# Optimization experiments

Hardware: AMD Instinct MI355X
Metric: run time of the kernel (lower is better)

The kernel has to match this reference:

```python
import jax, jax.numpy as jnp
import numpy as np

ALPHA = 0.2      # LeakyReLU negative slope
NEG_INF = -9e15  # mask value from the original code

def setup_inputs() -> dict:
    key = jax.random.key(0)
    k1, k2, k3, k4 = jax.random.split(key, 4)
    B, M, F_IN, F_OUT = 16, 2048, 128, 64
    h = jax.random.normal(k1, (B, M, F_IN), dtype=jnp.float32)
    adj = jax.random.randint(k2, (B, M, M), 0, 2, dtype=jnp.int32)
    W = jax.random.normal(k3, (F_IN, F_OUT), dtype=jnp.float32) * 0.1
    a = jax.random.normal(k4, (2 * F_OUT, 1), dtype=jnp.float32) * 0.1
    return {"h": h, "adj": adj, "W": W, "a": a}

def reference(h, adj, W, a):
    # h: [B,M,Fin], adj: [B,M,M], W: [Fin,E], a: [2E,1]
    Wh = jnp.matmul(h, W)                      # [B,M,E]
    E = Wh.shape[-1]
    a1, a2 = a[:E, 0], a[E:, 0]
    # decompose a^T [Wh_i || Wh_j] = (Wh_i . a1) + (Wh_j . a2)
    f1 = Wh @ a1                               # [B,M] (source/query term)
    f2 = Wh @ a2                               # [B,M] (target/key term)
    e = jax.nn.leaky_relu(f1[:, :, None] + f2[:, None, :], negative_slope=ALPHA)  # [B,M,M]
    scores = jnp.where(adj > 0, e, NEG_INF)
    attn = jax.nn.softmax(scores, axis=-1)     # [B,M,M]  (dropout p=0 / eval mode)
    h_prime = jnp.matmul(attn, Wh)             # [B,M,E]
    return jax.nn.elu(h_prime)                 # concat=True branch
```

## Files before the change

### kernel.cpp

```cpp
#include <hip/hip_runtime.h>


#define M_     2048
#define FIN_   128
#define F_     64
#define ALPHA_ 0.2f
#define ROWS_  64
#define TS_    36
#define WT_    132

typedef float  float4_ __attribute__((ext_vector_type(4)));
typedef short  short4_ __attribute__((ext_vector_type(4)));
typedef short  short8  __attribute__((ext_vector_type(8)));
typedef int    int4_   __attribute__((ext_vector_type(4)));
typedef unsigned short u16;
typedef unsigned int   u32;

static __device__ __forceinline__ float bf2f(u16 u) {
    return __uint_as_float(((u32)u) << 16);
}
static __device__ __forceinline__ u16 f2bf(float f) {
    u32 u = __float_as_uint(f);
    u32 r = u + 0x7FFFu + ((u >> 16) & 1u);
    return (u16)(r >> 16);
}

__global__ __launch_bounds__(512, 4) void k_gat3(
    const float* __restrict__ h, const int* __restrict__ adj,
    const float* __restrict__ W, const float* __restrict__ a,
    float* __restrict__ out)
{
    __shared__ u16   Wl[FIN_ * F_];
    __shared__ float a_s[2 * F_];
    __shared__ float wa1[FIN_], wa2[FIN_];
    __shared__ float f1s[ROWS_];
    __shared__ float dens[ROWS_];
    __shared__ char  dyn[WT_ * 64 * 4];

    u16*   hTbuf0 = (u16*)dyn;
    u16*   hTbuf1 = (u16*)(dyn + 9216);
    float* f2all  = (float*)(dyn + 18432);
    float* Tsum   = (float*)dyn;

    const int tid  = threadIdx.x;
    const int w    = tid >> 6;
    const int l    = tid & 63;
    const int lc   = l & 15;
    const int quad = l >> 4;
    const int b    = blockIdx.x >> 5;
    const int i0   = (blockIdx.x & 31) * ROWS_;

    if (tid < 128) a_s[tid] = a[tid];
    for (int e = tid; e < FIN_ * F_; e += 512) Wl[e] = f2bf(W[e]);
    __syncthreads();

    if (tid < FIN_) {
        float s1 = 0.f, s2 = 0.f;
#pragma unroll 8
        for (int n = 0; n < F_; ++n) {
            float wv = W[tid * F_ + n];
            s1 += wv * a_s[n];
            s2 += wv * a_s[F_ + n];
        }
        wa1[tid] = s1;
        wa2[tid] = s2;
    }
    __syncthreads();

    {
        const int r = tid >> 3, k0 = (tid & 7) * 16;
        const float* hp = h + ((size_t)(b * M_ + i0 + r)) * FIN_ + k0;
        float s = 0.f;
#pragma unroll
        for (int k = 0; k < 16; ++k) s += hp[k] * wa1[k0 + k];
        s += __shfl_xor(s, 1, 64);
        s += __shfl_xor(s, 2, 64);
        s += __shfl_xor(s, 4, 64);
        if ((tid & 7) == 0) f1s[r] = s;
    }

    {
        const int sf0 = (tid & 15) * 8;
        for (int p = 0; p < 64; ++p) {
            const int t = p * 32 + (tid >> 4);
            const float* hp = h + ((size_t)(b * M_ + t)) * FIN_ + sf0;
            float4_ x0 = *(const float4_*)hp;
            float4_ x1 = *(const float4_*)(hp + 4);
            float fp = 0.f;
            fp += x0[0] * wa2[sf0 + 0]; fp += x0[1] * wa2[sf0 + 1];
            fp += x0[2] * wa2[sf0 + 2]; fp += x0[3] * wa2[sf0 + 3];
            fp += x1[0] * wa2[sf0 + 4]; fp += x1[1] * wa2[sf0 + 5];
            fp += x1[2] * wa2[sf0 + 6]; fp += x1[3] * wa2[sf0 + 7];
            fp += __shfl_xor(fp, 1, 64);
            fp += __shfl_xor(fp, 2, 64);
            fp += __shfl_xor(fp, 4, 64);
            fp += __shfl_xor(fp, 8, 64);
            if ((tid & 15) == 0) f2all[t] = fp;
        }
    }

    const int rg  = w & 3;
    const int nh  = w >> 2;
    const int tq  = tid >> 5;
    const int f0  = (tid & 31) * 4;
    const int row = i0 + rg * 16 + lc;

    const int*   aprow  = adj + ((size_t)(b * M_ + row)) * M_ + quad * 8;
    const float* hstage = h + ((size_t)(b * M_ + 2 * tq)) * FIN_ + f0;

    int4_   aA0 = *(const int4_*)(aprow);
    int4_   aA1 = *(const int4_*)(aprow + 4);
    int4_   aB0 = *(const int4_*)(aprow + 32);
    int4_   aB1 = *(const int4_*)(aprow + 36);
    float4_ hA0 = *(const float4_*)(hstage);
    float4_ hA1 = *(const float4_*)(hstage + FIN_);

    __syncthreads();

    const float f1r = f1s[rg * 16 + lc];
    float denacc = 0.f;
    float4_ acc0 = {0.f,0.f,0.f,0.f}, acc1 = {0.f,0.f,0.f,0.f};
    float4_ acc2 = {0.f,0.f,0.f,0.f}, acc3 = {0.f,0.f,0.f,0.f};

    for (int t = 0; t < 64; ++t) {
        u16* hT = (t & 1) ? hTbuf1 : hTbuf0;
        const int j0 = t * 32;
        const int jn = (t < 63 ? t + 1 : 63) * 32;
        const int jp = (t < 62 ? t + 2 : 63) * 32;

        int4_   aC0 = *(const int4_*)(aprow + jp);
        int4_   aC1 = *(const int4_*)(aprow + jp + 4);
        float4_ hN0 = *(const float4_*)(hstage + (size_t)jn * FIN_);
        float4_ hN1 = *(const float4_*)(hstage + (size_t)jn * FIN_ + FIN_);

#pragma unroll
        for (int kk = 0; kk < 4; ++kk) {
            const int k   = f0 + kk;
            const int swz = (k >> 3) & 12;
            u32 pk = (u32)f2bf(hA0[kk]) | ((u32)f2bf(hA1[kk]) << 16);
            *(u32*)(hT + k * TS_ + 2 * (tq ^ swz)) = pk;
        }

        asm volatile("s_waitcnt lgkmcnt(0)" ::: "memory");
        __builtin_amdgcn_s_barrier();
        __builtin_amdgcn_sched_barrier(0);

        float4_ g0 = *(const float4_*)(f2all + j0 + quad * 8);
        float4_ g1 = *(const float4_*)(f2all + j0 + quad * 8 + 4);
        short8 af;
        float d = 0.f;
#define SCORE(J, GV, AV)                                   \
        {                                                  \
            float x_ = f1r + (GV);                         \
            x_ = fmaxf(x_, ALPHA_ * x_);                   \
            float e_ = ((AV) > 0) ? __expf(x_) : 0.f;      \
            u16 pb = f2bf(e_);                             \
            d += bf2f(pb);                                 \
            af[J] = (short)pb;                             \
        }
        SCORE(0, g0[0], aA0[0]) SCORE(1, g0[1], aA0[1])
        SCORE(2, g0[2], aA0[2]) SCORE(3, g0[3], aA0[3])
        SCORE(4, g1[0], aA1[0]) SCORE(5, g1[1], aA1[1])
        SCORE(6, g1[2], aA1[2]) SCORE(7, g1[3], aA1[3])
#undef SCORE
        denacc += d;

#define MTILE(C, ACC)                                                        \
        {                                                                    \
            const int fidx = (nh * 4 + (C)) * 16 + lc;                       \
            const int swzf = ((nh * 4 + (C)) * 2) & 12;                      \
            const u16* bp = hT + fidx * TS_ + (((quad * 4) ^ swzf) << 1);    \
            short4_ b0 = *(const short4_*)bp;                                \
            short4_ b1 = *(const short4_*)(bp + 4);                          \
            short8 bf;                                                       \
            bf[0] = b0[0]; bf[1] = b0[1]; bf[2] = b0[2]; bf[3] = b0[3];      \
            bf[4] = b1[0]; bf[5] = b1[1]; bf[6] = b1[2]; bf[7] = b1[3];      \
            ACC = __builtin_amdgcn_mfma_f32_16x16x32_bf16(af, bf, ACC, 0, 0, 0); \
        }
        MTILE(0, acc0) MTILE(1, acc1) MTILE(2, acc2) MTILE(3, acc3)
#undef MTILE

        aA0 = aB0; aA1 = aB1; aB0 = aC0; aB1 = aC1;
        hA0 = hN0; hA1 = hN1;
    }

    denacc += __shfl_xor(denacc, 16, 64);
    denacc += __shfl_xor(denacc, 32, 64);
    if (nh == 0 && quad == 0) dens[rg * 16 + lc] = denacc;
    __syncthreads();

#pragma unroll
    for (int mm = 0; mm < 4; ++mm) {
        const int rr = (rg * 16 + quad * 4 + mm) * WT_ + nh * 64 + lc;
        Tsum[rr +  0] = acc0[mm];
        Tsum[rr + 16] = acc1[mm];
        Tsum[rr + 32] = acc2[mm];
        Tsum[rr + 48] = acc3[mm];
    }
    __syncthreads();

    {
        const int r  = tid >> 3;
        const int n0 = (tid & 7) * 8;
        const float den  = dens[r];
        const float rden = (den > 0.f) ? (1.f / den) : 0.f;
        float u[8];
#pragma unroll
        for (int nn = 0; nn < 8; ++nn) u[nn] = 0.f;
        for (int k = 0; k < FIN_; ++k) {
            const float tv = Tsum[r * WT_ + k];
            short8 wv = *(const short8*)(Wl + k * F_ + n0);
#pragma unroll
            for (int nn = 0; nn < 8; ++nn) u[nn] += tv * bf2f((u16)wv[nn]);
        }
        float4_ o0, o1;
#pragma unroll
        for (int nn = 0; nn < 8; ++nn) {
            float hp = u[nn] * rden;
            float o  = hp > 0.f ? hp : expm1f(hp);
            if (nn < 4) o0[nn] = o; else o1[nn - 4] = o;
        }
        float* op = out + ((size_t)(b * M_ + i0 + r)) * F_ + n0;
        *(float4_*)op       = o0;
        *(float4_*)(op + 4) = o1;
    }
}

extern "C" void kernel_launch(void* const* d_in, const int* in_sizes, int n_in,
                              void* d_out, int out_size, void* d_ws, size_t ws_size,
                              hipStream_t stream)
{
    (void)out_size; (void)d_ws; (void)ws_size;
    const float* h  = (const float*)d_in[0];
    const int* adjp = (const int*)d_in[1];
    const float* Wp = (const float*)d_in[2];
    const float* ap = (const float*)d_in[3];
    for (int i = 0; i < n_in; ++i) {
        long s = in_sizes[i];
        if      (s == 4194304L)  h    = (const float*)d_in[i];
        else if (s == 67108864L) adjp = (const int*)d_in[i];
        else if (s == 8192L)     Wp   = (const float*)d_in[i];
        else if (s == 128L)      ap   = (const float*)d_in[i];
    }
    k_gat3<<<512, 512, 0, stream>>>(h, adjp, Wp, ap, (float*)d_out);
}
```

Baseline: 449.1 us.

## Halve rows per block, fuse f2 computation into tile loop, use packed bf16 converts

Each block now covers 32 rows with 256 threads across 1024 blocks, and block IDs are remapped to group batches. The up-front pass that computed f2 for all 2048 keys is removed; f2 for each 32-key tile is computed inside the main loop from the h values already staged, using double-buffered small LDS arrays. Manual bf16 rounding is replaced by v_cvt_pk_bf16_f32, adjacency prefetch goes one tile deeper, and the epilogue reads W in fp32 from global memory instead of a bf16 LDS copy. The aim is to remove the serial prologue and raise occupancy, at the cost of recomputing f2 and re-reading h per block.

```diff
diff --git a/kernel.cpp b/kernel.cpp
--- a/kernel.cpp
+++ b/kernel.cpp
@@ -5,7 +5,7 @@
 #define FIN_   128
 #define F_     64
 #define ALPHA_ 0.2f
-#define ROWS_  64
+#define ROWS_  32
 #define TS_    36
 #define WT_    132
 
@@ -13,33 +13,31 @@
 typedef short  short4_ __attribute__((ext_vector_type(4)));
 typedef short  short8  __attribute__((ext_vector_type(8)));
 typedef int    int4_   __attribute__((ext_vector_type(4)));
+typedef unsigned int u32x4 __attribute__((ext_vector_type(4)));
 typedef unsigned short u16;
 typedef unsigned int   u32;
 
-static __device__ __forceinline__ float bf2f(u16 u) {
-    return __uint_as_float(((u32)u) << 16);
+static __device__ __forceinline__ u32 cvtpk(float lo, float hi) {
+    u32 r;
+    asm("v_cvt_pk_bf16_f32 %0, %1, %2" : "=v"(r) : "v"(lo), "v"(hi));
+    return r;
 }
-static __device__ __forceinline__ u16 f2bf(float f) {
-    u32 u = __float_as_uint(f);
-    u32 r = u + 0x7FFFu + ((u >> 16) & 1u);
-    return (u16)(r >> 16);
-}
-
-__global__ __launch_bounds__(512, 4) void k_gat3(
+
+__global__ __launch_bounds__(256, 4) void k_gat4(
     const float* __restrict__ h, const int* __restrict__ adj,
     const float* __restrict__ W, const float* __restrict__ a,
     float* __restrict__ out)
 {
-    __shared__ u16   Wl[FIN_ * F_];
     __shared__ float a_s[2 * F_];
     __shared__ float wa1[FIN_], wa2[FIN_];
     __shared__ float f1s[ROWS_];
     __shared__ float dens[ROWS_];
-    __shared__ char  dyn[WT_ * 64 * 4];
+    __shared__ char  dyn[18688];
 
     u16*   hTbuf0 = (u16*)dyn;
     u16*   hTbuf1 = (u16*)(dyn + 9216);
-    float* f2all  = (float*)(dyn + 18432);
+    float* f2t0   = (float*)(dyn + 18432);
+    float* f2t1   = (float*)(dyn + 18560);
     float* Tsum   = (float*)dyn;
 
     const int tid  = threadIdx.x;
@@ -47,11 +45,18 @@
     const int l    = tid & 63;
     const int lc   = l & 15;
     const int quad = l >> 4;
-    const int b    = blockIdx.x >> 5;
-    const int i0   = (blockIdx.x & 31) * ROWS_;
+
+    const u32 bid = blockIdx.x;
+    const u32 lg  = (bid & 7) * 128 + (bid >> 3);
+    const int b   = lg >> 6;
+    const int i0  = (lg & 63) * ROWS_;
+
+    const int rg = w & 1;
+    const int nh = w >> 1;
+    const int fo = tid & 15;
+    const int tp = tid >> 4;
 
     if (tid < 128) a_s[tid] = a[tid];
-    for (int e = tid; e < FIN_ * F_; e += 512) Wl[e] = f2bf(W[e]);
     __syncthreads();
 
     if (tid < FIN_) {
@@ -79,41 +84,22 @@
         if ((tid & 7) == 0) f1s[r] = s;
     }
 
-    {
-        const int sf0 = (tid & 15) * 8;
-        for (int p = 0; p < 64; ++p) {
-            const int t = p * 32 + (tid >> 4);
-            const float* hp = h + ((size_t)(b * M_ + t)) * FIN_ + sf0;
-            float4_ x0 = *(const float4_*)hp;
-            float4_ x1 = *(const float4_*)(hp + 4);
-            float fp = 0.f;
-            fp += x0[0] * wa2[sf0 + 0]; fp += x0[1] * wa2[sf0 + 1];
-            fp += x0[2] * wa2[sf0 + 2]; fp += x0[3] * wa2[sf0 + 3];
-            fp += x1[0] * wa2[sf0 + 4]; fp += x1[1] * wa2[sf0 + 5];
-            fp += x1[2] * wa2[sf0 + 6]; fp += x1[3] * wa2[sf0 + 7];
-            fp += __shfl_xor(fp, 1, 64);
-            fp += __shfl_xor(fp, 2, 64);
-            fp += __shfl_xor(fp, 4, 64);
-            fp += __shfl_xor(fp, 8, 64);
-            if ((tid & 15) == 0) f2all[t] = fp;
-        }
-    }
-
-    const int rg  = w & 3;
-    const int nh  = w >> 2;
-    const int tq  = tid >> 5;
-    const int f0  = (tid & 31) * 4;
-    const int row = i0 + rg * 16 + lc;
-
-    const int*   aprow  = adj + ((size_t)(b * M_ + row)) * M_ + quad * 8;
-    const float* hstage = h + ((size_t)(b * M_ + 2 * tq)) * FIN_ + f0;
+    float4_ w2a = *(const float4_*)(wa2 + fo * 8);
+    float4_ w2b = *(const float4_*)(wa2 + fo * 8 + 4);
+
+    const int*   aprow  = adj + ((size_t)(b * M_ + i0 + rg * 16 + lc)) * M_ + quad * 8;
+    const float* hstage = h + ((size_t)(b * M_ + 2 * tp)) * FIN_ + fo * 8;
 
     int4_   aA0 = *(const int4_*)(aprow);
     int4_   aA1 = *(const int4_*)(aprow + 4);
     int4_   aB0 = *(const int4_*)(aprow + 32);
     int4_   aB1 = *(const int4_*)(aprow + 36);
-    float4_ hA0 = *(const float4_*)(hstage);
-    float4_ hA1 = *(const float4_*)(hstage + FIN_);
+    int4_   aC0 = *(const int4_*)(aprow + 64);
+    int4_   aC1 = *(const int4_*)(aprow + 68);
+    float4_ hE0 = *(const float4_*)(hstage);
+    float4_ hE1 = *(const float4_*)(hstage + 4);
+    float4_ hO0 = *(const float4_*)(hstage + FIN_);
+    float4_ hO1 = *(const float4_*)(hstage + FIN_ + 4);
 
     __syncthreads();
 
@@ -122,66 +108,82 @@
     float4_ acc0 = {0.f,0.f,0.f,0.f}, acc1 = {0.f,0.f,0.f,0.f};
     float4_ acc2 = {0.f,0.f,0.f,0.f}, acc3 = {0.f,0.f,0.f,0.f};
 
+#pragma unroll 2
     for (int t = 0; t < 64; ++t) {
-        u16* hT = (t & 1) ? hTbuf1 : hTbuf0;
-        const int j0 = t * 32;
+        u16*   hT  = (t & 1) ? hTbuf1 : hTbuf0;
+        float* f2c = (t & 1) ? f2t1   : f2t0;
         const int jn = (t < 63 ? t + 1 : 63) * 32;
-        const int jp = (t < 62 ? t + 2 : 63) * 32;
-
-        int4_   aC0 = *(const int4_*)(aprow + jp);
-        int4_   aC1 = *(const int4_*)(aprow + jp + 4);
-        float4_ hN0 = *(const float4_*)(hstage + (size_t)jn * FIN_);
-        float4_ hN1 = *(const float4_*)(hstage + (size_t)jn * FIN_ + FIN_);
-
-#pragma unroll
-        for (int kk = 0; kk < 4; ++kk) {
-            const int k   = f0 + kk;
-            const int swz = (k >> 3) & 12;
-            u32 pk = (u32)f2bf(hA0[kk]) | ((u32)f2bf(hA1[kk]) << 16);
-            *(u32*)(hT + k * TS_ + 2 * (tq ^ swz)) = pk;
+        const int jp = (t < 61 ? t + 3 : 63) * 32;
+
+        int4_   nA0 = *(const int4_*)(aprow + jp);
+        int4_   nA1 = *(const int4_*)(aprow + jp + 4);
+        float4_ nE0 = *(const float4_*)(hstage + (size_t)jn * FIN_);
+        float4_ nE1 = *(const float4_*)(hstage + (size_t)jn * FIN_ + 4);
+        float4_ nO0 = *(const float4_*)(hstage + (size_t)jn * FIN_ + FIN_);
+        float4_ nO1 = *(const float4_*)(hstage + (size_t)jn * FIN_ + FIN_ + 4);
+
+        {
+            u16* wbase = hT + fo * (8 * TS_) + 2 * (tp ^ (fo & 12));
+            float fp0 = 0.f, fp1 = 0.f;
+#pragma unroll
+            for (int kk = 0; kk < 8; ++kk) {
+                float ev = (kk < 4) ? hE0[kk] : hE1[kk - 4];
+                float od = (kk < 4) ? hO0[kk] : hO1[kk - 4];
+                *(u32*)(wbase + kk * TS_) = cvtpk(ev, od);
+                float wk = (kk < 4) ? w2a[kk] : w2b[kk - 4];
+                fp0 += ev * wk;
+                fp1 += od * wk;
+            }
+            fp0 += __shfl_xor(fp0, 1, 64); fp1 += __shfl_xor(fp1, 1, 64);
+            fp0 += __shfl_xor(fp0, 2, 64); fp1 += __shfl_xor(fp1, 2, 64);
+            fp0 += __shfl_xor(fp0, 4, 64); fp1 += __shfl_xor(fp1, 4, 64);
+            fp0 += __shfl_xor(fp0, 8, 64); fp1 += __shfl_xor(fp1, 8, 64);
+            if (fo == 0) { f2c[2 * tp] = fp0; f2c[2 * tp + 1] = fp1; }
         }
 
         asm volatile("s_waitcnt lgkmcnt(0)" ::: "memory");
         __builtin_amdgcn_s_barrier();
         __builtin_amdgcn_sched_barrier(0);
 
-        float4_ g0 = *(const float4_*)(f2all + j0 + quad * 8);
-        float4_ g1 = *(const float4_*)(f2all + j0 + quad * 8 + 4);
-        short8 af;
+        float4_ g0 = *(const float4_*)(f2c + quad * 8);
+        float4_ g1 = *(const float4_*)(f2c + quad * 8 + 4);
+        u32x4 pw;
         float d = 0.f;
-#define SCORE(J, GV, AV)                                   \
-        {                                                  \
-            float x_ = f1r + (GV);                         \
-            x_ = fmaxf(x_, ALPHA_ * x_);                   \
-            float e_ = ((AV) > 0) ? __expf(x_) : 0.f;      \
-            u16 pb = f2bf(e_);                             \
-            d += bf2f(pb);                                 \
-            af[J] = (short)pb;                             \
-        }
-        SCORE(0, g0[0], aA0[0]) SCORE(1, g0[1], aA0[1])
-        SCORE(2, g0[2], aA0[2]) SCORE(3, g0[3], aA0[3])
-        SCORE(4, g1[0], aA1[0]) SCORE(5, g1[1], aA1[1])
-        SCORE(6, g1[2], aA1[2]) SCORE(7, g1[3], aA1[3])
-#undef SCORE
+#define SC(GE, GO, AE, AO, IDX)                                 \
+        {                                                       \
+            float xe = f1r + (GE); xe = fmaxf(xe, ALPHA_ * xe); \
+            float xo = f1r + (GO); xo = fmaxf(xo, ALPHA_ * xo); \
+            float ee = ((AE) > 0) ? __expf(xe) : 0.f;           \
+            float eo = ((AO) > 0) ? __expf(xo) : 0.f;           \
+            u32 pk = cvtpk(ee, eo);                             \
+            d += __uint_as_float(pk << 16);                     \
+            d += __uint_as_float(pk & 0xFFFF0000u);             \
+            pw[IDX] = pk;                                       \
+        }
+        SC(g0[0], g0[1], aA0[0], aA0[1], 0)
+        SC(g0[2], g0[3], aA0[2], aA0[3], 1)
+        SC(g1[0], g1[1], aA1[0], aA1[1], 2)
+        SC(g1[2], g1[3], aA1[2], aA1[3], 3)
+#undef SC
         denacc += d;
-
-#define MTILE(C, ACC)                                                        \
-        {                                                                    \
-            const int fidx = (nh * 4 + (C)) * 16 + lc;                       \
-            const int swzf = ((nh * 4 + (C)) * 2) & 12;                      \
-            const u16* bp = hT + fidx * TS_ + (((quad * 4) ^ swzf) << 1);    \
-            short4_ b0 = *(const short4_*)bp;                                \
-            short4_ b1 = *(const short4_*)(bp + 4);                          \
-            short8 bf;                                                       \
-            bf[0] = b0[0]; bf[1] = b0[1]; bf[2] = b0[2]; bf[3] = b0[3];      \
-            bf[4] = b1[0]; bf[5] = b1[1]; bf[6] = b1[2]; bf[7] = b1[3];      \
+        short8 af = __builtin_bit_cast(short8, pw);
+
+#define MT(C, ACC)                                                             \
+        {                                                                      \
+            const u16* bp = hT + ((nh * 4 + (C)) * 16 + lc) * TS_              \
+                          + (((quad * 4) ^ (((nh * 4 + (C)) * 2) & 12)) << 1); \
+            short4_ b0 = *(const short4_*)bp;                                  \
+            short4_ b1 = *(const short4_*)(bp + 4);                            \
+            short8 bf;                                                         \
+            bf[0] = b0[0]; bf[1] = b0[1]; bf[2] = b0[2]; bf[3] = b0[3];        \
+            bf[4] = b1[0]; bf[5] = b1[1]; bf[6] = b1[2]; bf[7] = b1[3];        \
             ACC = __builtin_amdgcn_mfma_f32_16x16x32_bf16(af, bf, ACC, 0, 0, 0); \
         }
-        MTILE(0, acc0) MTILE(1, acc1) MTILE(2, acc2) MTILE(3, acc3)
-#undef MTILE
-
-        aA0 = aB0; aA1 = aB1; aB0 = aC0; aB1 = aC1;
-        hA0 = hN0; hA1 = hN1;
+        MT(0, acc0) MT(1, acc1) MT(2, acc2) MT(3, acc3)
+#undef MT
+
+        aA0 = aB0; aA1 = aB1; aB0 = aC0; aB1 = aC1; aC0 = nA0; aC1 = nA1;
+        hE0 = nE0; hE1 = nE1; hO0 = nO0; hO1 = nO1;
     }
 
     denacc += __shfl_xor(denacc, 16, 64);
@@ -191,11 +193,11 @@
 
 #pragma unroll
     for (int mm = 0; mm < 4; ++mm) {
-        const int rr = (rg * 16 + quad * 4 + mm) * WT_ + nh * 64 + lc;
-        Tsum[rr +  0] = acc0[mm];
-        Tsum[rr + 16] = acc1[mm];
-        Tsum[rr + 32] = acc2[mm];
-        Tsum[rr + 48] = acc3[mm];
+        float* tr = Tsum + (rg * 16 + quad * 4 + mm) * WT_ + nh * 64 + lc;
+        tr[0]  = acc0[mm];
+        tr[16] = acc1[mm];
+        tr[32] = acc2[mm];
+        tr[48] = acc3[mm];
     }
     __syncthreads();
 
@@ -207,11 +209,15 @@
         float u[8];
 #pragma unroll
         for (int nn = 0; nn < 8; ++nn) u[nn] = 0.f;
+#pragma unroll 4
         for (int k = 0; k < FIN_; ++k) {
             const float tv = Tsum[r * WT_ + k];
-            short8 wv = *(const short8*)(Wl + k * F_ + n0);
-#pragma unroll
-            for (int nn = 0; nn < 8; ++nn) u[nn] += tv * bf2f((u16)wv[nn]);
+            float4_ wv0 = *(const float4_*)(W + k * F_ + n0);
+            float4_ wv1 = *(const float4_*)(W + k * F_ + n0 + 4);
+            u[0] += tv * wv0[0]; u[1] += tv * wv0[1];
+            u[2] += tv * wv0[2]; u[3] += tv * wv0[3];
+            u[4] += tv * wv1[0]; u[5] += tv * wv1[1];
+            u[6] += tv * wv1[2]; u[7] += tv * wv1[3];
         }
         float4_ o0, o1;
 #pragma unroll
@@ -242,5 +248,5 @@
         else if (s == 8192L)     Wp   = (const float*)d_in[i];
         else if (s == 128L)      ap   = (const float*)d_in[i];
     }
-    k_gat3<<<512, 512, 0, stream>>>(h, adjp, Wp, ap, (float*)d_out);
+    k_gat4<<<1024, 256, 0, stream>>>(h, adjp, Wp, ap, (float*)d_out);
 }
```

New measurement: 483.5 us. 7.7% more time.
